# Performance work log

Hardware: AMD Instinct MI355X
Metric: run time of the kernel (lower is better)

## Reference

```python
import jax, jax.numpy as jnp
import numpy as np

N = 10000


def gcn_conv(x, W, b, src, dst, n):
    """GCNConv: linear transform then symmetric-normalized aggregation with self-loops."""
    h = x @ W  # [n, out]
    loops = jnp.arange(n, dtype=src.dtype)
    s = jnp.concatenate([src, loops])
    d = jnp.concatenate([dst, loops])
    deg = jnp.zeros((n,), h.dtype).at[d].add(1.0)
    dinv = jax.lax.rsqrt(jnp.maximum(deg, 1.0))
    norm = dinv[s] * dinv[d]  # [E+n]
    out = jax.ops.segment_sum(h[s] * norm[:, None], d, num_segments=n)
    return out + b


def aggr(x1, x2, aw):
    """TwoOrderAggrConv: learned per-channel softmax combine of the two orders."""
    w = jax.nn.softmax(aw, axis=1)  # [C, 2]
    return x1 * w[:, 0] + x2 * w[:, 1]


def setup_inputs() -> dict:
    key = jax.random.key(0)
    ks = jax.random.split(key, 16)

    def glorot(k, shape):
        fan_in, fan_out = shape
        lim = np.sqrt(6.0 / (fan_in + fan_out)).astype(np.float32)
        return jax.random.uniform(k, shape, jnp.float32, -lim, lim)

    inp = {
        'node_feature': jax.random.normal(ks[0], (N, 512), jnp.float32),
        'edge_index1': jax.random.randint(ks[1], (2, 80000), 0, N, jnp.int32),
        'edge_index2': jax.random.randint(ks[2], (2, 160000), 0, N, jnp.int32),
        'W11': glorot(ks[3], (512, 1024)), 'b11': jnp.zeros((1024,), jnp.float32),
        'W12': glorot(ks[4], (512, 1024)), 'b12': jnp.zeros((1024,), jnp.float32),
        'W21': glorot(ks[5], (1024, 512)), 'b21': jnp.zeros((512,), jnp.float32),
        'W22': glorot(ks[6], (1024, 512)), 'b22': jnp.zeros((512,), jnp.float32),
        'W31': glorot(ks[7], (512, 128)), 'b31': jnp.zeros((128,), jnp.float32),
        'W32': glorot(ks[8], (512, 128)), 'b32': jnp.zeros((128,), jnp.float32),
        'aw1': jax.random.normal(ks[9], (1024, 2), jnp.float32) * 0.1,
        'aw2': jax.random.normal(ks[10], (512, 2), jnp.float32) * 0.1,
        'aw3': jax.random.normal(ks[11], (128, 2), jnp.float32) * 0.1,
    }
    return inp


def reference(node_feature, edge_index1, edge_index2,
              W11, b11, W12, b12, W21, b21, W22, b22, W31, b31, W32, b32,
              aw1, aw2, aw3):
    n = node_feature.shape[0]
    s1, d1 = edge_index1[0], edge_index1[1]
    s2, d2 = edge_index2[0], edge_index2[1]
    # dropout in eval mode -> identity
    h1 = jax.nn.elu(gcn_conv(node_feature, W11, b11, s1, d1, n))
    h2 = jax.nn.elu(gcn_conv(node_feature, W12, b12, s2, d2, n))
    h = aggr(h1, h2, aw1)
    h1 = jax.nn.elu(gcn_conv(h, W21, b21, s1, d1, n))
    h2 = jax.nn.elu(gcn_conv(h, W22, b22, s2, d2, n))
    h = aggr(h1, h2, aw2)
    h1 = jax.nn.elu(gcn_conv(h, W31, b31, s1, d1, n))
    h2 = jax.nn.elu(gcn_conv(h, W32, b32, s2, d2, n))
    return aggr(h1, h2, aw3)
```

## Files before the change

kernel.cpp:

```cpp
#include <hip/hip_runtime.h>
#include <hip/hip_bf16.h>
#include <math.h>

using bf16 = __hip_bfloat16;
typedef __attribute__((ext_vector_type(8))) short short8;
typedef __attribute__((ext_vector_type(4))) float floatx4;

__device__ inline void gl_lds16(const void* g, void* l) {
  __builtin_amdgcn_global_load_lds(
      (const __attribute__((address_space(1))) unsigned int*)g,
      (__attribute__((address_space(3))) unsigned int*)l,
      16, 0, 0);
}
__device__ inline float eluf(float x) { return x > 0.f ? x : __expf(x) - 1.f; }
__device__ inline float bf2f(unsigned short h) {
  return __uint_as_float(((unsigned)h) << 16);
}
__device__ inline void bf16x8_fma(short8 r, float w, float* acc) {
#pragma unroll
  for (int k = 0; k < 8; k++) acc[k] += w * bf2f((unsigned short)r[k]);
}

__global__ void probe_zero(const unsigned short* __restrict__ x, int* __restrict__ flag,
                           int* __restrict__ zbase, int zwords) {
  if (blockIdx.x == 0) {
    __shared__ int s;
    int t = threadIdx.x;
    if (t == 0) s = 0;
    __syncthreads();
    int bad = 0;
    for (int i = t; i < 1024; i += 256) {
      unsigned short h = x[2 * i];
      unsigned e = (h >> 7) & 0xFF;
      if (e >= 0xE5) bad = 1;
    }
    if (bad) atomicOr(&s, 1);
    __syncthreads();
    if (t == 0) flag[0] = s;
  } else {
    int i = (blockIdx.x - 1) * 1024 + threadIdx.x * 4;
    if (i < zwords) {
      zbase[i] = 0; zbase[i + 1] = 0; zbase[i + 2] = 0; zbase[i + 3] = 0;
    }
  }
}

__global__ void prep_all(
    const void* X, bf16* __restrict__ Xb, int nx,
    const void* W11, const void* W12, const void* W21, const void* W22,
    const void* W31, const void* W32,
    bf16* Wt11, bf16* Wt12, bf16* Wt2cat, bf16* Wt3cat,
    const void* b11, const void* b12, const void* b21, const void* b22,
    const void* b31, const void* b32, const void* aw1, const void* aw2, const void* aw3,
    float* ob11, float* ob12, float* ob21, float* ob22, float* ob31, float* ob32,
    float* ow1, float* ow2, float* ow3,
    const int* __restrict__ dst1, int E1, const int* __restrict__ dst2, int E2,
    int* __restrict__ deg1, int* __restrict__ deg2,
    const int* __restrict__ flag) {
  const bool f32 = *flag != 0;
  int b = blockIdx.x;
  const int xbBlocks = nx / 2048;
  if (b < 2176) {
    __shared__ bf16 tile[32][33];
    const void* in; bf16* out; int K, N, tt;
    if (b < 512)       { in = W11; out = Wt11; K = 512;  N = 1024; tt = b; }
    else if (b < 1024) { in = W12; out = Wt12; K = 512;  N = 1024; tt = b - 512; }
    else if (b < 1536) { in = W21; out = Wt2cat; K = 1024; N = 512; tt = b - 1024; }
    else if (b < 2048) { in = W22; out = Wt2cat + (size_t)512 * 1024; K = 1024; N = 512; tt = b - 1536; }
    else if (b < 2112) { in = W31; out = Wt3cat; K = 512; N = 128; tt = b - 2048; }
    else               { in = W32; out = Wt3cat + (size_t)128 * 512; K = 512; N = 128; tt = b - 2112; }
    int tilesx = N / 32;
    int bx = (tt % tilesx) * 32;
    int by = (tt / tilesx) * 32;
    int tx = threadIdx.x & 31, ty = threadIdx.x >> 5;
#pragma unroll
    for (int i = 0; i < 32; i += 8) {
      size_t idx = (size_t)(by + ty + i) * N + (bx + tx);
      tile[ty + i][tx] = f32 ? __float2bfloat16(((const float*)in)[idx])
                             : ((const bf16*)in)[idx];
    }
    __syncthreads();
#pragma unroll
    for (int i = 0; i < 32; i += 8)
      out[(size_t)(bx + ty + i) * K + (by + tx)] = tile[tx][ty + i];
    return;
  }
  b -= 2176;
  if (b < xbBlocks) {
    int e = (b * 256 + threadIdx.x) * 8;
    if (f32) {
      const float* src = (const float*)X + e;
      short8 r;
#pragma unroll
      for (int k = 0; k < 8; k++)
        r[k] = (short)__bfloat16_as_ushort(__float2bfloat16(src[k]));
      *(short8*)(Xb + e) = r;
    } else {
      *(short8*)(Xb + e) = *(const short8*)((const bf16*)X + e);
    }
    return;
  }
  b -= xbBlocks;
  if (b < 20) {
    auto cv = [&](const void* p, int i) -> float {
      return f32 ? ((const float*)p)[i] : __bfloat162float(((const bf16*)p)[i]);
    };
    int t = b * 256 + threadIdx.x;
    if (t < 1024) ob11[t] = cv(b11, t);
    else if (t < 2048) ob12[t - 1024] = cv(b12, t - 1024);
    else if (t < 2560) ob21[t - 2048] = cv(b21, t - 2048);
    else if (t < 3072) ob22[t - 2560] = cv(b22, t - 2560);
    else if (t < 3200) ob31[t - 3072] = cv(b31, t - 3072);
    else if (t < 3328) ob32[t - 3200] = cv(b32, t - 3200);
    else if (t < 4992) {
      int j = t - 3328;
      const void* src; float* dst; int jj;
      if (j < 1024)      { src = aw1; dst = ow1; jj = j; }
      else if (j < 1536) { src = aw2; dst = ow2; jj = j - 1024; }
      else               { src = aw3; dst = ow3; jj = j - 1536; }
      float e0 = cv(src, 2 * jj), e1 = cv(src, 2 * jj + 1);
      float mx = fmaxf(e0, e1);
      float w0 = expf(e0 - mx), w1 = expf(e1 - mx);
      float inv = 1.f / (w0 + w1);
      dst[2 * jj] = w0 * inv;
      dst[2 * jj + 1] = w1 * inv;
    }
    return;
  }
  b -= 20;
  {
    int e = b * 256 + threadIdx.x;
    if (e < E1) atomicAdd(&deg1[dst1[e]], 1);
    else if (e < E1 + E2) atomicAdd(&deg2[dst2[e - E1]], 1);
  }
}

__global__ void scan2_kernel(const int* __restrict__ deg1, int* __restrict__ off1,
                             float* __restrict__ dinv1,
                             const int* __restrict__ deg2, int* __restrict__ off2,
                             float* __restrict__ dinv2, int n) {
  const int* deg = blockIdx.x ? deg2 : deg1;
  int* off = blockIdx.x ? off2 : off1;
  float* dinv = blockIdx.x ? dinv2 : dinv1;
  __shared__ int wsum[16];
  __shared__ int carry_s;
  const int t = threadIdx.x;
  const int waveid = t >> 6;
  const int lane = t & 63;
  if (t == 0) carry_s = 0;
  __syncthreads();
  for (int base = 0; base < n; base += 1024) {
    int i = base + t;
    int orig = (i < n) ? deg[i] : 0;
    int v = orig;
#pragma unroll
    for (int d = 1; d < 64; d <<= 1) {
      int u = __shfl_up(v, d, 64);
      if (lane >= d) v += u;
    }
    if (lane == 63) wsum[waveid] = v;
    __syncthreads();
    if (waveid == 0 && lane < 16) {
      int s = wsum[lane];
#pragma unroll
      for (int d = 1; d < 16; d <<= 1) {
        int u = __shfl_up(s, d, 64);
        if (lane >= d) s += u;
      }
      wsum[lane] = s;
    }
    __syncthreads();
    int woff = waveid ? wsum[waveid - 1] : 0;
    int incl = v + woff;
    int carry = carry_s;
    if (i < n) {
      off[i]  = carry + incl - orig;
      dinv[i] = rsqrtf((float)(orig + 1));
    }
    __syncthreads();
    if (t == 1023) carry_s = carry + wsum[15];
    __syncthreads();
  }
  if (t == 0) off[n] = carry_s;
}

__global__ void csr_fused(const int* __restrict__ src1, const int* __restrict__ dst1, int E1,
                          const int* __restrict__ src2, const int* __restrict__ dst2, int E2,
                          const int* __restrict__ off1, int* __restrict__ cur1,
                          const float* __restrict__ dinv1,
                          int* __restrict__ cs1, float* __restrict__ cw1,
                          const int* __restrict__ off2, int* __restrict__ cur2,
                          const float* __restrict__ dinv2,
                          int* __restrict__ cs2, float* __restrict__ cw2) {
  int e = blockIdx.x * 256 + threadIdx.x;
  if (e < E1) {
    int d = dst1[e], s = src1[e];
    int slot = off1[d] + atomicAdd(&cur1[d], 1);
    cs1[slot] = s;
    cw1[slot] = dinv1[s];
  } else if (e < E1 + E2) {
    int ee = e - E1;
    int d = dst2[ee], s = src2[ee];
    int slot = off2[d] + atomicAdd(&cur2[d], 1);
    cs2[slot] = s;
    cw2[slot] = dinv2[s];
  }
}

template <int LD>
__device__ inline void gather_accum(const bf16* __restrict__ base,
                                    const int* __restrict__ cs, const float* __restrict__ cw,
                                    int s, int e, float* acc) {
  int i = s;
  for (; i + 8 <= e; i += 8) {
    short8 r[8]; float w[8];
#pragma unroll
    for (int k = 0; k < 8; k++) {
      r[k] = *(const short8*)(base + (size_t)cs[i + k] * LD);
      w[k] = cw[i + k];
    }
#pragma unroll
    for (int k = 0; k < 8; k++) bf16x8_fma(r[k], w[k], acc);
  }
  for (; i + 4 <= e; i += 4) {
    short8 r[4]; float w[4];
#pragma unroll
    for (int k = 0; k < 4; k++) {
      r[k] = *(const short8*)(base + (size_t)cs[i + k] * LD);
      w[k] = cw[i + k];
    }
#pragma unroll
    for (int k = 0; k < 4; k++) bf16x8_fma(r[k], w[k], acc);
  }
  for (; i + 2 <= e; i += 2) {
    short8 r0 = *(const short8*)(base + (size_t)cs[i] * LD);
    short8 r1 = *(const short8*)(base + (size_t)cs[i + 1] * LD);
    bf16x8_fma(r0, cw[i], acc);
    bf16x8_fma(r1, cw[i + 1], acc);
  }
  if (i < e) {
    short8 r0 = *(const short8*)(base + (size_t)cs[i] * LD);
    bf16x8_fma(r0, cw[i], acc);
  }
}

__global__ __launch_bounds__(256) void aggx_kernel(
    const bf16* __restrict__ X,
    const int* __restrict__ off1, const int* __restrict__ cs1, const float* __restrict__ cw1,
    const int* __restrict__ off2, const int* __restrict__ cs2, const float* __restrict__ cw2,
    const float* __restrict__ dinv1, const float* __restrict__ dinv2,
    bf16* __restrict__ outA, bf16* __restrict__ outB, int n) {
  int v = blockIdx.x * 4 + (threadIdx.x >> 6);
  if (v >= n) return;
  v = __builtin_amdgcn_readfirstlane(v);
  const int c = (threadIdx.x & 63) * 8;
  const bf16* __restrict__ base = X + c;

  float a[8], b[8];
#pragma unroll
  for (int k = 0; k < 8; k++) { a[k] = 0.f; b[k] = 0.f; }

  int s1 = __builtin_amdgcn_readfirstlane(off1[v]);
  int e1 = __builtin_amdgcn_readfirstlane(off1[v + 1]);
  gather_accum<512>(base, cs1, cw1, s1, e1, a);
  int s2 = __builtin_amdgcn_readfirstlane(off2[v]);
  int e2 = __builtin_amdgcn_readfirstlane(off2[v + 1]);
  gather_accum<512>(base, cs2, cw2, s2, e2, b);

  short8 self = *(const short8*)(base + (size_t)v * 512);
  const float dv1 = dinv1[v], dv2 = dinv2[v];
  short8 ra, rb;
#pragma unroll
  for (int k = 0; k < 8; k++) {
    float xs = bf2f((unsigned short)self[k]);
    ra[k] = (short)__bfloat16_as_ushort(__float2bfloat16(dv1 * a[k] + dv1 * dv1 * xs));
    rb[k] = (short)__bfloat16_as_ushort(__float2bfloat16(dv2 * b[k] + dv2 * dv2 * xs));
  }
  *(short8*)(outA + (size_t)v * 512 + c) = ra;
  *(short8*)(outB + (size_t)v * 512 + c) = rb;
}

__device__ inline void gemm_body(const bf16* __restrict__ A, const bf16* __restrict__ Bt,
                                 bf16* __restrict__ C, int M, int K, int N,
                                 int m0, int n0) {
  __shared__ bf16 As[128 * 32];
  __shared__ bf16 Bs[128 * 32];
  const int tid = threadIdx.x;
  const int wave = tid >> 6;
  const int lane = tid & 63;
  const int quad = lane >> 4;
  const int l16 = lane & 15;
  const int wr = (wave >> 1) * 64;
  const int wc = (wave & 1) * 64;
  const int r_sub = lane >> 2;
  const int cb = (((lane & 3) ^ ((lane >> 3) & 3)) * 16);
  const int rsw = (l16 >> 1) & 3;

  floatx4 acc[4][4];
#pragma unroll
  for (int i = 0; i < 4; i++)
#pragma unroll
    for (int j = 0; j < 4; j++) acc[i][j] = (floatx4){0.f, 0.f, 0.f, 0.f};

  for (int k0 = 0; k0 < K; k0 += 32) {
    __syncthreads();
#pragma unroll
    for (int j = 0; j < 2; ++j) {
      int p = wave * 2 + j;
      int ra = p * 16 + r_sub;
      int grow = m0 + ra; if (grow >= M) grow = M - 1;
      gl_lds16((const char*)(A + (size_t)grow * K + k0) + cb, (char*)As + p * 1024);
      int rb = n0 + p * 16 + r_sub;
      gl_lds16((const char*)(Bt + (size_t)rb * K + k0) + cb, (char*)Bs + p * 1024);
    }
    __syncthreads();

    short8 af[4], bfr[4];
#pragma unroll
    for (int i = 0; i < 4; i++)
      af[i] = *(const short8*)(As + (wr + i * 16 + l16) * 32 + (quad ^ rsw) * 8);
#pragma unroll
    for (int j = 0; j < 4; j++)
      bfr[j] = *(const short8*)(Bs + (wc + j * 16 + l16) * 32 + (quad ^ rsw) * 8);
#pragma unroll
    for (int i = 0; i < 4; i++)
#pragma unroll
      for (int j = 0; j < 4; j++)
        acc[i][j] = __builtin_amdgcn_mfma_f32_16x16x32_bf16(af[i], bfr[j], acc[i][j], 0, 0, 0);
  }

#pragma unroll
  for (int i = 0; i < 4; i++) {
#pragma unroll
    for (int r = 0; r < 4; r++) {
      int row = m0 + wr + i * 16 + quad * 4 + r;
      if (row < M) {
#pragma unroll
        for (int j = 0; j < 4; j++) {
          int col = n0 + wc + j * 16 + l16;
          C[(size_t)row * N + col] = __float2bfloat16(acc[i][j][r]);
        }
      }
    }
  }
}

__global__ __launch_bounds__(256) void gemm128_sw(
    const bf16* __restrict__ A0, const bf16* __restrict__ Bt0, bf16* __restrict__ C0,
    const bf16* __restrict__ A1, const bf16* __restrict__ Bt1, bf16* __restrict__ C1,
    int M, int K, int N, int mtilesPerHalf, int mtTotal, int ntLog2) {
  int lin = blockIdx.x;
  int g = lin & 7;
  int s = lin >> 3;
  int n_t = s & ((1 << ntLog2) - 1);
  int m_t = g + 8 * (s >> ntLog2);
  if (m_t >= mtTotal) return;
  int half = (m_t >= mtilesPerHalf) ? 1 : 0;
  int m_local = m_t - half * mtilesPerHalf;
  const bf16* A = half ? A1 : A0;
  const bf16* Bt = half ? Bt1 : Bt0;
  bf16* C = half ? C1 : C0;
  gemm_body(A, Bt, C, M, K, N, m_local * 128, n_t * 128);
}

__global__ __launch_bounds__(256) void combine1_kernel(
    const bf16* __restrict__ Ha, const bf16* __restrict__ Hb,
    const float* __restrict__ ba, const float* __restrict__ bb,
    const float* __restrict__ w01, bf16* __restrict__ out, int total) {
  int e = (blockIdx.x * 256 + threadIdx.x) * 8;
  if (e >= total) return;
  int c = e & 1023;
  short8 ha = *(const short8*)(Ha + e);
  short8 hb = *(const short8*)(Hb + e);
  short8 r;
#pragma unroll
  for (int k = 0; k < 8; k++) {
    float x = eluf(bf2f((unsigned short)ha[k]) + ba[c + k]);
    float y = eluf(bf2f((unsigned short)hb[k]) + bb[c + k]);
    r[k] = (short)__bfloat16_as_ushort(
        __float2bfloat16(x * w01[2 * (c + k)] + y * w01[2 * (c + k) + 1]));
  }
  *(short8*)(out + e) = r;
}

template <int C, int LD, bool WU>
__global__ __launch_bounds__(256) void agg_out_kernel(
    const bf16* __restrict__ Ha, const bf16* __restrict__ Hb,
    const int* __restrict__ off1, const int* __restrict__ cs1, const float* __restrict__ cw1,
    const int* __restrict__ off2, const int* __restrict__ cs2, const float* __restrict__ cw2,
    const float* __restrict__ dinv1, const float* __restrict__ dinv2,
    const float* __restrict__ ba, const float* __restrict__ bb,
    const float* __restrict__ w01, void* __restrict__ out, int n,
    const int* __restrict__ outflag) {
  constexpr int TPV = C / 8;
  constexpr int G = 256 / TPV;
  const int t = threadIdx.x;
  int v = blockIdx.x * G + t / TPV;
  if (v >= n) return;
  if (WU) v = __builtin_amdgcn_readfirstlane(v);
  const int c = (t % TPV) * 8;
  const bf16* __restrict__ baseA = Ha + c;
  const bf16* __restrict__ baseB = Hb + c;

  float a[8], b[8];
#pragma unroll
  for (int k = 0; k < 8; k++) { a[k] = 0.f; b[k] = 0.f; }

  int s1 = off1[v], e1 = off1[v + 1];
  if (WU) { s1 = __builtin_amdgcn_readfirstlane(s1); e1 = __builtin_amdgcn_readfirstlane(e1); }
  gather_accum<LD>(baseA, cs1, cw1, s1, e1, a);
  int s2 = off2[v], e2 = off2[v + 1];
  if (WU) { s2 = __builtin_amdgcn_readfirstlane(s2); e2 = __builtin_amdgcn_readfirstlane(e2); }
  gather_accum<LD>(baseB, cs2, cw2, s2, e2, b);

  short8 sa = *(const short8*)(baseA + (size_t)v * LD);
  short8 sb = *(const short8*)(baseB + (size_t)v * LD);
  const float dv1 = dinv1[v], dv2 = dinv2[v];

  float r[8];
#pragma unroll
  for (int k = 0; k < 8; k++) {
    float x = eluf(dv1 * a[k] + dv1 * dv1 * bf2f((unsigned short)sa[k]) + ba[c + k]);
    float y = eluf(dv2 * b[k] + dv2 * dv2 * bf2f((unsigned short)sb[k]) + bb[c + k]);
    r[k] = x * w01[2 * (c + k)] + y * w01[2 * (c + k) + 1];
  }

  const bool out_f32 = (outflag != nullptr) && (*outflag != 0);
  size_t oi = (size_t)v * C + c;
  if (out_f32) {
    floatx4 lo = {r[0], r[1], r[2], r[3]};
    floatx4 hi = {r[4], r[5], r[6], r[7]};
    *(floatx4*)((float*)out + oi) = lo;
    *(floatx4*)((float*)out + oi + 4) = hi;
  } else {
    short8 rb;
#pragma unroll
    for (int k = 0; k < 8; k++)
      rb[k] = (short)__bfloat16_as_ushort(__float2bfloat16(r[k]));
    *(short8*)((bf16*)out + oi) = rb;
  }
}

extern "C" void kernel_launch(void* const* d_in, const int* in_sizes, int n_in,
                              void* d_out, int out_size, void* d_ws, size_t ws_size,
                              hipStream_t stream) {
  const void* X = d_in[0];
  const int* ei1 = (const int*)d_in[1];
  const int* ei2 = (const int*)d_in[2];
  const int n = in_sizes[0] / 512;
  const int E1 = in_sizes[1] / 2;
  const int E2 = in_sizes[2] / 2;
  const int* src1 = ei1;           const int* dst1 = ei1 + E1;
  const int* src2 = ei2;           const int* dst2 = ei2 + E2;

  auto rnd = [](size_t b) { return (b + 255) & ~(size_t)255; };
  char* p = (char*)d_ws;
  auto alloc = [&](size_t bytes) { char* r = p; p += rnd(bytes); return r; };

  int* flag = (int*)alloc(256);
  int* deg1 = (int*)alloc((size_t)n * 4);
  int* deg2 = (int*)alloc((size_t)n * 4);
  int* cur1 = (int*)alloc((size_t)n * 4);
  int* cur2 = (int*)alloc((size_t)n * 4);
  int* off1 = (int*)alloc((size_t)(n + 1) * 4);
  int* off2 = (int*)alloc((size_t)(n + 1) * 4);
  float* dinv1 = (float*)alloc((size_t)n * 4);
  float* dinv2 = (float*)alloc((size_t)n * 4);
  int* cs1 = (int*)alloc((size_t)E1 * 4);
  float* cw1 = (float*)alloc((size_t)E1 * 4);
  int* cs2 = (int*)alloc((size_t)E2 * 4);
  float* cw2 = (float*)alloc((size_t)E2 * 4);
  bf16* Wt11 = (bf16*)alloc((size_t)512 * 1024 * 2);
  bf16* Wt12 = (bf16*)alloc((size_t)512 * 1024 * 2);
  bf16* Wt2cat = (bf16*)alloc((size_t)1024 * 1024 * 2);
  bf16* Wt3cat = (bf16*)alloc((size_t)256 * 512 * 2);
  float* bf_[6]; int bsz[6] = {1024, 1024, 512, 512, 128, 128};
  for (int i = 0; i < 6; i++) bf_[i] = (float*)alloc((size_t)bsz[i] * 4);
  float* w01_[3]; int asz[3] = {2048, 1024, 256};
  for (int i = 0; i < 3; i++) w01_[i] = (float*)alloc((size_t)asz[i] * 4);
  bf16* Xb = (bf16*)alloc((size_t)n * 512 * 2);
  bf16* aggXa = (bf16*)alloc((size_t)n * 512 * 2);
  bf16* aggXb = (bf16*)alloc((size_t)n * 512 * 2);
  bf16* H1a = (bf16*)alloc((size_t)n * 1024 * 2);
  bf16* H1b = (bf16*)alloc((size_t)n * 1024 * 2);
  bf16* act1 = (bf16*)alloc((size_t)n * 1024 * 2);
  bf16* H2cat = H1a;
  bf16* act2 = aggXa;
  bf16* H3cat = H1b;

  int zwords = (int)(rnd((size_t)n * 4) * 4 / 4);
  probe_zero<<<1 + (zwords + 1023) / 1024, 256, 0, stream>>>(
      (const unsigned short*)X, flag, deg1, zwords);

  int xbBlocks = (n * 512) / 2048;
  int degBlocks = (E1 + E2 + 255) / 256;
  prep_all<<<2176 + xbBlocks + 20 + degBlocks, 256, 0, stream>>>(
      X, Xb, n * 512,
      d_in[3], d_in[5], d_in[7], d_in[9], d_in[11], d_in[13],
      Wt11, Wt12, Wt2cat, Wt3cat,
      d_in[4], d_in[6], d_in[8], d_in[10], d_in[12], d_in[14],
      d_in[15], d_in[16], d_in[17],
      bf_[0], bf_[1], bf_[2], bf_[3], bf_[4], bf_[5],
      w01_[0], w01_[1], w01_[2],
      dst1, E1, dst2, E2, deg1, deg2, flag);

  scan2_kernel<<<2, 1024, 0, stream>>>(deg1, off1, dinv1, deg2, off2, dinv2, n);
  csr_fused<<<(E1 + E2 + 255) / 256, 256, 0, stream>>>(src1, dst1, E1, src2, dst2, E2,
                                                       off1, cur1, dinv1, cs1, cw1,
                                                       off2, cur2, dinv2, cs2, cw2);

  const int mtiles = (n + 127) / 128;
  auto swgrid = [](int mtTotal, int ntiles) {
    return 8 * ntiles * ((mtTotal + 7) / 8);
  };
  aggx_kernel<<<(n + 3) / 4, 256, 0, stream>>>(Xb, off1, cs1, cw1, off2, cs2, cw2,
                                               dinv1, dinv2, aggXa, aggXb, n);
  gemm128_sw<<<swgrid(2 * mtiles, 8), 256, 0, stream>>>(
      aggXa, Wt11, H1a, aggXb, Wt12, H1b, n, 512, 1024, mtiles, 2 * mtiles, 3);
  combine1_kernel<<<(n * 1024 / 8 + 255) / 256, 256, 0, stream>>>(
      H1a, H1b, bf_[0], bf_[1], w01_[0], act1, n * 1024);
  gemm128_sw<<<swgrid(mtiles, 8), 256, 0, stream>>>(
      act1, Wt2cat, H2cat, act1, Wt2cat, H2cat, n, 1024, 1024, mtiles, mtiles, 3);
  agg_out_kernel<512, 1024, true><<<(n + 3) / 4, 256, 0, stream>>>(
      H2cat, H2cat + 512, off1, cs1, cw1, off2, cs2, cw2,
      dinv1, dinv2, bf_[2], bf_[3], w01_[1], act2, n, (const int*)nullptr);
  gemm128_sw<<<swgrid(mtiles, 2), 256, 0, stream>>>(
      act2, Wt3cat, H3cat, act2, Wt3cat, H3cat, n, 512, 256, mtiles, mtiles, 1);
  agg_out_kernel<128, 256, false><<<(n + 15) / 16, 256, 0, stream>>>(
      H3cat, H3cat + 128, off1, cs1, cw1, off2, cs2, cw2,
      dinv1, dinv2, bf_[4], bf_[5], w01_[2], d_out, n, flag);
}
```

Before: 316.7 us.

## Fuse layer-1 dual GEMM with bias, ELU and softmax combine epilogue

Replaces the layer-1 paired GEMM plus separate combine kernel with one kernel that computes both GEMMs on the same output tile (128x64) and applies bias, ELU and the learned two-way weighting in the epilogue, writing act1 directly. This removes the write and re-read of two n x 1024 bf16 intermediates and one launch. In exchange the new GEMM uses a smaller N tile, no double-buffering, and scattered per-element 2-byte stores, so its efficiency may be lower than the tuned gemm128 path.

```diff
diff --git a/kernel.cpp b/kernel.cpp
--- a/kernel.cpp
+++ b/kernel.cpp
@@ -363,24 +363,99 @@
   gemm_body(A, Bt, C, M, K, N, m_local * 128, n_t * 128);
 }
 
-__global__ __launch_bounds__(256) void combine1_kernel(
-    const bf16* __restrict__ Ha, const bf16* __restrict__ Hb,
+__global__ __launch_bounds__(256) void gemm_l1f(
+    const bf16* __restrict__ Aa, const bf16* __restrict__ Bta,
+    const bf16* __restrict__ Ab, const bf16* __restrict__ Btb,
     const float* __restrict__ ba, const float* __restrict__ bb,
-    const float* __restrict__ w01, bf16* __restrict__ out, int total) {
-  int e = (blockIdx.x * 256 + threadIdx.x) * 8;
-  if (e >= total) return;
-  int c = e & 1023;
-  short8 ha = *(const short8*)(Ha + e);
-  short8 hb = *(const short8*)(Hb + e);
-  short8 r;
-#pragma unroll
-  for (int k = 0; k < 8; k++) {
-    float x = eluf(bf2f((unsigned short)ha[k]) + ba[c + k]);
-    float y = eluf(bf2f((unsigned short)hb[k]) + bb[c + k]);
-    r[k] = (short)__bfloat16_as_ushort(
-        __float2bfloat16(x * w01[2 * (c + k)] + y * w01[2 * (c + k) + 1]));
-  }
-  *(short8*)(out + e) = r;
+    const float* __restrict__ w01, bf16* __restrict__ out,
+    int M, int K, int N, int mtiles) {
+  int lin = blockIdx.x;
+  int g = lin & 7;
+  int s = lin >> 3;
+  int n_t = s & 15;
+  int m_t = g + 8 * (s >> 4);
+  if (m_t >= mtiles) return;
+  const int m0 = m_t * 128, n0 = n_t * 64;
+
+  __shared__ bf16 Asa[128 * 32];
+  __shared__ bf16 Asb[128 * 32];
+  __shared__ bf16 Bsa[64 * 32];
+  __shared__ bf16 Bsb[64 * 32];
+  const int tid = threadIdx.x;
+  const int wave = tid >> 6;
+  const int lane = tid & 63;
+  const int quad = lane >> 4;
+  const int l16 = lane & 15;
+  const int wr = (wave >> 1) * 64;
+  const int wc = (wave & 1) * 32;
+  const int r_sub = lane >> 2;
+  const int cb = (((lane & 3) ^ ((lane >> 3) & 3)) * 16);
+  const int rsw = (l16 >> 1) & 3;
+
+  floatx4 acca[4][2], accb[4][2];
+#pragma unroll
+  for (int i = 0; i < 4; i++)
+#pragma unroll
+    for (int j = 0; j < 2; j++) {
+      acca[i][j] = (floatx4){0.f, 0.f, 0.f, 0.f};
+      accb[i][j] = (floatx4){0.f, 0.f, 0.f, 0.f};
+    }
+
+  for (int k0 = 0; k0 < K; k0 += 32) {
+    __syncthreads();
+#pragma unroll
+    for (int j = 0; j < 2; ++j) {
+      int p = wave * 2 + j;
+      int ra = p * 16 + r_sub;
+      int grow = m0 + ra; if (grow >= M) grow = M - 1;
+      gl_lds16((const char*)(Aa + (size_t)grow * K + k0) + cb, (char*)Asa + p * 1024);
+      gl_lds16((const char*)(Ab + (size_t)grow * K + k0) + cb, (char*)Asb + p * 1024);
+    }
+    {
+      int rb = n0 + wave * 16 + r_sub;
+      gl_lds16((const char*)(Bta + (size_t)rb * K + k0) + cb, (char*)Bsa + wave * 1024);
+      gl_lds16((const char*)(Btb + (size_t)rb * K + k0) + cb, (char*)Bsb + wave * 1024);
+    }
+    __syncthreads();
+
+    short8 afa[4], afb[4], bfa[2], bfb[2];
+#pragma unroll
+    for (int i = 0; i < 4; i++) {
+      afa[i] = *(const short8*)(Asa + (wr + i * 16 + l16) * 32 + (quad ^ rsw) * 8);
+      afb[i] = *(const short8*)(Asb + (wr + i * 16 + l16) * 32 + (quad ^ rsw) * 8);
+    }
+#pragma unroll
+    for (int j = 0; j < 2; j++) {
+      bfa[j] = *(const short8*)(Bsa + (wc + j * 16 + l16) * 32 + (quad ^ rsw) * 8);
+      bfb[j] = *(const short8*)(Bsb + (wc + j * 16 + l16) * 32 + (quad ^ rsw) * 8);
+    }
+#pragma unroll
+    for (int i = 0; i < 4; i++)
+#pragma unroll
+      for (int j = 0; j < 2; j++) {
+        acca[i][j] = __builtin_amdgcn_mfma_f32_16x16x32_bf16(afa[i], bfa[j], acca[i][j], 0, 0, 0);
+        accb[i][j] = __builtin_amdgcn_mfma_f32_16x16x32_bf16(afb[i], bfb[j], accb[i][j], 0, 0, 0);
+      }
+  }
+
+#pragma unroll
+  for (int j = 0; j < 2; j++) {
+    int col = n0 + wc + j * 16 + l16;
+    float baj = ba[col], bbj = bb[col];
+    float w0 = w01[2 * col], w1 = w01[2 * col + 1];
+#pragma unroll
+    for (int i = 0; i < 4; i++) {
+#pragma unroll
+      for (int r = 0; r < 4; r++) {
+        int row = m0 + wr + i * 16 + quad * 4 + r;
+        if (row < M) {
+          float x = eluf(acca[i][j][r] + baj);
+          float y = eluf(accb[i][j][r] + bbj);
+          out[(size_t)row * N + col] = __float2bfloat16(x * w0 + y * w1);
+        }
+      }
+    }
+  }
 }
 
 template <int C, int LD, bool WU>
@@ -482,11 +557,10 @@
   bf16* aggXa = (bf16*)alloc((size_t)n * 512 * 2);
   bf16* aggXb = (bf16*)alloc((size_t)n * 512 * 2);
   bf16* H1a = (bf16*)alloc((size_t)n * 1024 * 2);
-  bf16* H1b = (bf16*)alloc((size_t)n * 1024 * 2);
   bf16* act1 = (bf16*)alloc((size_t)n * 1024 * 2);
   bf16* H2cat = H1a;
   bf16* act2 = aggXa;
-  bf16* H3cat = H1b;
+  bf16* H3cat = aggXb;
 
   int zwords = (int)(rnd((size_t)n * 4) * 4 / 4);
   probe_zero<<<1 + (zwords + 1023) / 1024, 256, 0, stream>>>(
@@ -515,10 +589,8 @@
   };
   aggx_kernel<<<(n + 3) / 4, 256, 0, stream>>>(Xb, off1, cs1, cw1, off2, cs2, cw2,
                                                dinv1, dinv2, aggXa, aggXb, n);
-  gemm128_sw<<<swgrid(2 * mtiles, 8), 256, 0, stream>>>(
-      aggXa, Wt11, H1a, aggXb, Wt12, H1b, n, 512, 1024, mtiles, 2 * mtiles, 3);
-  combine1_kernel<<<(n * 1024 / 8 + 255) / 256, 256, 0, stream>>>(
-      H1a, H1b, bf_[0], bf_[1], w01_[0], act1, n * 1024);
+  gemm_l1f<<<swgrid(mtiles, 16), 256, 0, stream>>>(
+      aggXa, Wt11, aggXb, Wt12, bf_[0], bf_[1], w01_[0], act1, n, 512, 1024, mtiles);
   gemm128_sw<<<swgrid(mtiles, 8), 256, 0, stream>>>(
       act1, Wt2cat, H2cat, act1, Wt2cat, H2cat, n, 1024, 1024, mtiles, mtiles, 3);
   agg_out_kernel<512, 1024, true><<<(n + 3) / 4, 256, 0, stream>>>(
```

Result: no change. 313.9 us (-0.9%).
